# Kernel optimization log

Hardware: AMD Instinct MI355X
Metric: run time of the kernel (lower is better)

The kernel has to match this reference:

```python
import jax, jax.numpy as jnp
import numpy as np

B, L, D = 64, 512, 768          # batch, BERT seq len, BERT hidden
J = 31                          # clause boundaries per doc
S = J + 1                       # clauses per doc (= decoder max_len)
H = 100                         # enc/dec GRU hidden
NC = 10                         # num label classes
EMB = 50                        # label embedding dim


def setup_inputs() -> dict:
    key = jax.random.key(0)
    ks = jax.random.split(key, 24)
    sc = 0.05
    hidden_state = jax.random.normal(ks[0], (B, L, D), jnp.float32)
    # strictly increasing, non-zero boundaries -> every clause slice is non-empty
    stride = L // S  # 16
    bert_clause_b = jnp.tile(((jnp.arange(J) + 1) * stride)[None, :], (B, 1)).astype(jnp.int32)
    p = dict(
        hidden_state=hidden_state,
        bert_clause_b=bert_clause_b,
        fc5_w=sc * jax.random.normal(ks[1], (D, 1), jnp.float32),
        fc5_b=jnp.zeros((1,), jnp.float32),
        # encoder bi-GRU (input 768 -> hidden 100), torch gate order r,z,n
        enc_wih_f=sc * jax.random.normal(ks[2], (3 * H, D), jnp.float32),
        enc_whh_f=sc * jax.random.normal(ks[3], (3 * H, H), jnp.float32),
        enc_bih_f=jnp.zeros((3 * H,), jnp.float32),
        enc_bhh_f=jnp.zeros((3 * H,), jnp.float32),
        enc_wih_b=sc * jax.random.normal(ks[4], (3 * H, D), jnp.float32),
        enc_whh_b=sc * jax.random.normal(ks[5], (3 * H, H), jnp.float32),
        enc_bih_b=jnp.zeros((3 * H,), jnp.float32),
        enc_bhh_b=jnp.zeros((3 * H,), jnp.float32),
        emb=sc * jax.random.normal(ks[6], (NC, EMB), jnp.float32),
        lin1_w=sc * jax.random.normal(ks[7], (H, 2 * H), jnp.float32),
        lin1_b=jnp.zeros((H,), jnp.float32),
        dec_wih=sc * jax.random.normal(ks[8], (3 * H, EMB + H), jnp.float32),
        dec_whh=sc * jax.random.normal(ks[9], (3 * H, H), jnp.float32),
        dec_bih=jnp.zeros((3 * H,), jnp.float32),
        dec_bhh=jnp.zeros((3 * H,), jnp.float32),
        h2l_w=sc * jax.random.normal(ks[10], (NC, H), jnp.float32),
        h2l_b=jnp.zeros((NC,), jnp.float32),
    )
    return p


def _gru_cell(x, h, wih, whh, bih, bhh):
    gi = x @ wih.T + bih
    gh = h @ whh.T + bhh
    gir, giz, gin = jnp.split(gi, 3, axis=-1)
    ghr, ghz, ghn = jnp.split(gh, 3, axis=-1)
    r = jax.nn.sigmoid(gir + ghr)
    z = jax.nn.sigmoid(giz + ghz)
    n = jnp.tanh(gin + r * ghn)
    return (1.0 - z) * n + z * h


def _gru_scan(xs, h0, wih, whh, bih, bhh):
    # xs: [T, B, I]
    def step(h, x):
        h2 = _gru_cell(x, h, wih, whh, bih, bhh)
        return h2, h2
    return jax.lax.scan(step, h0, xs)


def reference(hidden_state, bert_clause_b, fc5_w, fc5_b,
              enc_wih_f, enc_whh_f, enc_bih_f, enc_bhh_f,
              enc_wih_b, enc_whh_b, enc_bih_b, enc_bhh_b,
              emb, lin1_w, lin1_b, dec_wih, dec_whh, dec_bih, dec_bhh,
              h2l_w, h2l_b):
    # ---- batched_index_select: per-clause softmax-weighted pooling ----
    t = jnp.arange(L)
    seg_id = jnp.sum(t[None, :, None] >= bert_clause_b[:, None, :], axis=-1)  # [B, L]
    scores = jnp.squeeze(hidden_state @ fc5_w, -1) + fc5_b[0]                  # [B, L]
    mask = seg_id[:, None, :] == jnp.arange(S)[None, :, None]                  # [B, S, L]
    logits = jnp.where(mask, scores[:, None, :], -jnp.inf)
    w = jax.nn.softmax(logits, axis=-1)                                        # [B, S, L]
    doc = jnp.einsum('bsl,bld->bsd', w, hidden_state)                          # [B, S, D]

    # ---- encoder bi-GRU ----
    xs = doc.transpose(1, 0, 2)  # [S, B, D]
    h0 = jnp.zeros((B, H), jnp.float32)
    hT_f, ys_f = _gru_scan(xs, h0, enc_wih_f, enc_whh_f, enc_bih_f, enc_bhh_f)
    _, ys_b = _gru_scan(xs[::-1], h0, enc_wih_b, enc_whh_b, enc_bih_b, enc_bhh_b)
    output1 = jnp.concatenate([ys_f, ys_b[::-1]], axis=-1)  # [S, B, 2H]

    # ---- decoder (greedy / testing=True path) ----
    lin = output1 @ lin1_w.T + lin1_b  # [S, B, H]

    def dec_step(carry, lin_t):
        h, prev = carry
        x = jnp.concatenate([emb[prev], lin_t], axis=-1)  # [B, EMB+H]
        h2 = _gru_cell(x, h, dec_wih, dec_whh, dec_bih, dec_bhh)
        logp = jax.nn.log_softmax(h2 @ h2l_w.T + h2l_b, axis=-1)  # [B, NC]
        nxt = jnp.argmax(logp, axis=-1).astype(jnp.int32)
        return (h2, nxt), logp

    init = (hT_f, jnp.zeros((B,), jnp.int32))
    _, outputs = jax.lax.scan(dec_step, init, lin)
    return outputs  # [S, B, NC] log-probs
```

## Files before the change

kernel.cpp:

```cpp
#include <hip/hip_runtime.h>
#include <hip/hip_bf16.h>
#include <math.h>

#define B_ 64
#define L_ 512
#define D_ 768
#define J_ 31
#define S_ 32
#define H_ 100
#define G3 300
#define NC_ 10
#define EMB_ 50

__device__ __forceinline__ float sigmoidf_(float x) { return 1.0f / (1.0f + __expf(-x)); }
__device__ __forceinline__ float tanhf_(float x) {
    float e = __expf(2.0f * x);
    return 1.0f - 2.0f / (e + 1.0f);
}
__device__ __forceinline__ float dot4f_(float4 a, float4 b) {
    return a.x * b.x + a.y * b.y + a.z * b.z + a.w * b.w;
}

typedef _Float16 half2_t __attribute__((ext_vector_type(2)));
__device__ __forceinline__ half2_t u_as_h2(unsigned u) { return __builtin_bit_cast(half2_t, u); }
__device__ __forceinline__ unsigned packh2(float a, float b) {
    half2_t p; p.x = (_Float16)a; p.y = (_Float16)b;
    return __builtin_bit_cast(unsigned, p);
}

__global__ __launch_bounds__(256) void pool_prep_kernel(
    const float* __restrict__ hs, const int* __restrict__ cb,
    const float* __restrict__ fc5w, const float* __restrict__ fc5b,
    float* __restrict__ doc,
    const float* __restrict__ dwih, const float* __restrict__ l1w,
    const float* __restrict__ l1b, const float* __restrict__ emb,
    const float* __restrict__ bih,
    float* __restrict__ W2, float* __restrict__ b2, float* __restrict__ tcg,
    const float* __restrict__ ewhf, const float* __restrict__ ewhb,
    const float* __restrict__ dwhh, unsigned* __restrict__ wpack)
{
    __shared__ __align__(16) float acc_s[4][D_];
    __shared__ float m_s[4], l_s[4];

    int bidx = blockIdx.x;
    int tid = threadIdx.x;

    if (bidx >= 2048) {
        if (bidx < 2348) {
            int n = bidx - 2048;
            __shared__ float dw_s[H_];
            int k = tid;
            if (k < H_) dw_s[k] = dwih[(size_t)n * 150 + 50 + k];
            __syncthreads();
            if (k < 200) {
                float acc = 0.f;
                for (int i = 0; i < H_; ++i) acc += dw_s[i] * l1w[(size_t)i * 200 + k];
                W2[(size_t)n * 200 + k] = acc;
            } else if (k == 200) {
                float acc = 0.f;
                for (int i = 0; i < H_; ++i) acc += dw_s[i] * l1b[i];
                b2[n] = acc;
            } else if (k < 211) {
                int c = k - 201;
                float acc = bih[n];
                const float* er = emb + c * EMB_;
                const float* wr = dwih + (size_t)n * 150;
                for (int e = 0; e < EMB_; ++e) acc += er[e] * wr[e];
                tcg[c * G3 + n] = acc;
            }
        } else {
            int m = bidx - 2348;
            const float* whh = (m == 0) ? ewhf : (m == 1) ? ewhb : dwhh;
            for (int t = tid; t < 400; t += 256) {
                int j = t >> 2, q = t & 3;
                unsigned* o = wpack + (size_t)m * 16000 + (size_t)t * 40;
#pragma unroll
                for (int d = 0; d < 13; ++d) {
                    int k = 2 * (13 * q + d);
                    float r0 = (k < H_) ? whh[j * H_ + k] : 0.f;
                    float r1 = (k + 1 < H_) ? whh[j * H_ + k + 1] : 0.f;
                    float z0 = (k < H_) ? whh[(100 + j) * H_ + k] : 0.f;
                    float z1 = (k + 1 < H_) ? whh[(100 + j) * H_ + k + 1] : 0.f;
                    float n0 = (k < H_) ? whh[(200 + j) * H_ + k] : 0.f;
                    float n1 = (k + 1 < H_) ? whh[(200 + j) * H_ + k + 1] : 0.f;
                    o[d]      = packh2(r0, r1);
                    o[13 + d] = packh2(z0, z1);
                    o[26 + d] = packh2(n0, n1);
                }
                o[39] = 0u;
            }
        }
        return;
    }

    int s = bidx >> 6, b = bidx & 63;
    int start = (s == 0) ? 0 : cb[b * J_ + s - 1];
    int end   = (s == J_) ? L_ : cb[b * J_ + s];
    int nt = end - start;
    int lane = tid & 63, wv = tid >> 6;

    if (nt <= 0) {
        for (int d = tid; d < D_; d += 256) doc[((size_t)s * B_ + b) * D_ + d] = 0.f;
        return;
    }

    float4 fwv[3];
#pragma unroll
    for (int i = 0; i < 3; ++i)
        fwv[i] = *(const float4*)(fc5w + 4 * lane + 256 * i);
    float bias = fc5b[0];

    const float* base = hs + ((size_t)b * L_ + start) * D_;
    float m = -INFINITY, l = 0.f;
    float4 acc[3];
#pragma unroll
    for (int i = 0; i < 3; ++i) acc[i] = make_float4(0.f, 0.f, 0.f, 0.f);

    for (int t = wv; t < nt; t += 4) {
        const float* row = base + (size_t)t * D_;
        float4 x0 = *(const float4*)(row + 4 * lane);
        float4 x1 = *(const float4*)(row + 4 * lane + 256);
        float4 x2 = *(const float4*)(row + 4 * lane + 512);
        float p = dot4f_(x0, fwv[0]) + dot4f_(x1, fwv[1]) + dot4f_(x2, fwv[2]);
#pragma unroll
        for (int off = 32; off; off >>= 1) p += __shfl_xor(p, off);
        p += bias;
        if (p > m) {
            float sc = __expf(m - p);
            l *= sc;
#pragma unroll
            for (int i = 0; i < 3; ++i) {
                acc[i].x *= sc; acc[i].y *= sc; acc[i].z *= sc; acc[i].w *= sc;
            }
            m = p;
        }
        float e = __expf(p - m);
        l += e;
        acc[0].x += e * x0.x; acc[0].y += e * x0.y; acc[0].z += e * x0.z; acc[0].w += e * x0.w;
        acc[1].x += e * x1.x; acc[1].y += e * x1.y; acc[1].z += e * x1.z; acc[1].w += e * x1.w;
        acc[2].x += e * x2.x; acc[2].y += e * x2.y; acc[2].z += e * x2.z; acc[2].w += e * x2.w;
    }
#pragma unroll
    for (int i = 0; i < 3; ++i)
        *(float4*)&acc_s[wv][4 * lane + 256 * i] = acc[i];
    if (lane == 0) { m_s[wv] = m; l_s[wv] = l; }
    __syncthreads();

    float M = fmaxf(fmaxf(m_s[0], m_s[1]), fmaxf(m_s[2], m_s[3]));
    float f0 = (l_s[0] > 0.f) ? __expf(m_s[0] - M) : 0.f;
    float f1 = (l_s[1] > 0.f) ? __expf(m_s[1] - M) : 0.f;
    float f2 = (l_s[2] > 0.f) ? __expf(m_s[2] - M) : 0.f;
    float f3 = (l_s[3] > 0.f) ? __expf(m_s[3] - M) : 0.f;
    float inv = 1.f / (l_s[0] * f0 + l_s[1] * f1 + l_s[2] * f2 + l_s[3] * f3);
    float* o = doc + ((size_t)s * B_ + b) * D_;
#pragma unroll
    for (int i = 0; i < 3; ++i) {
        int d = tid + 256 * i;
        float num = acc_s[0][d] * f0 + acc_s[1][d] * f1
                  + acc_s[2][d] * f2 + acc_s[3][d] * f3;
        o[d] = num * inv;
    }
}

__global__ __launch_bounds__(256) void gemm_enc(
    const float* __restrict__ A,
    const float* __restrict__ Wf, const float* __restrict__ Wb,
    const float* __restrict__ bf_, const float* __restrict__ bb_,
    float* __restrict__ C)
{
    __shared__ __align__(16) unsigned As[16][68];
    __shared__ __align__(16) unsigned Ws[16][68];
    int n0 = blockIdx.x * 64, m0 = blockIdx.y * 64;
    int tid = threadIdx.x;
    int tx = tid & 15, ty = tid >> 4;
    int lr = tid >> 2, lk4 = tid & 3;
    float acc[4][4] = {};

    for (int kk = 0; kk < 384; kk += 16) {
        {
            const float* ap = A + ((size_t)(m0 + lr)) * D_ + (kk + lk4 * 4) * 2;
            float4 x = *(const float4*)ap;
            float4 y = *(const float4*)(ap + 4);
            As[lk4 * 4 + 0][lr] = packh2(x.x, x.y);
            As[lk4 * 4 + 1][lr] = packh2(x.z, x.w);
            As[lk4 * 4 + 2][lr] = packh2(y.x, y.y);
            As[lk4 * 4 + 3][lr] = packh2(y.z, y.w);
            int n = n0 + lr;
            float4 u = make_float4(0.f, 0.f, 0.f, 0.f);
            float4 v = make_float4(0.f, 0.f, 0.f, 0.f);
            if (n < G3) {
                const float* wp = Wf + (size_t)n * D_ + (kk + lk4 * 4) * 2;
                u = *(const float4*)wp; v = *(const float4*)(wp + 4);
            } else if (n < 600) {
                const float* wp = Wb + (size_t)(n - G3) * D_ + (kk + lk4 * 4) * 2;
                u = *(const float4*)wp; v = *(const float4*)(wp + 4);
            }
            Ws[lk4 * 4 + 0][lr] = packh2(u.x, u.y);
            Ws[lk4 * 4 + 1][lr] = packh2(u.z, u.w);
            Ws[lk4 * 4 + 2][lr] = packh2(v.x, v.y);
            Ws[lk4 * 4 + 3][lr] = packh2(v.z, v.w);
        }
        __syncthreads();
#pragma unroll
        for (int ku = 0; ku < 16; ++ku) {
            uint4 av = *(const uint4*)&As[ku][ty * 4];
            uint4 wv = *(const uint4*)&Ws[ku][tx * 4];
            unsigned aa[4] = {av.x, av.y, av.z, av.w};
            unsigned ww[4] = {wv.x, wv.y, wv.z, wv.w};
#pragma unroll
            for (int i = 0; i < 4; ++i)
#pragma unroll
                for (int jj = 0; jj < 4; ++jj)
                    acc[i][jj] = __builtin_amdgcn_fdot2(u_as_h2(aa[i]), u_as_h2(ww[jj]),
                                                        acc[i][jj], false);
        }
        __syncthreads();
    }
#pragma unroll
    for (int jj = 0; jj < 4; ++jj) {
        int n = n0 + tx * 4 + jj;
        if (n >= 600) continue;
        float bias = (n < G3) ? bf_[n] : bb_[n - G3];
#pragma unroll
        for (int i = 0; i < 4; ++i) {
            int m = m0 + ty * 4 + i;
            C[(size_t)m * 600 + n] = acc[i][jj] + bias;
        }
    }
}

__global__ __launch_bounds__(256) void gemm_gil(
    const float* __restrict__ A, const float* __restrict__ W,
    const float* __restrict__ bias, float* __restrict__ C)
{
    __shared__ __align__(16) float As[16][68];
    __shared__ __align__(16) float Ws[16][68];
    int n0 = blockIdx.x * 64, m0 = blockIdx.y * 64;
    int tid = threadIdx.x;
    int tx = tid & 15, ty = tid >> 4;
    int lr = tid >> 2, lk4 = tid & 3;
    float acc[4][4] = {};

    for (int kk = 0; kk < 208; kk += 16) {
        int k = kk + lk4 * 4;
        float4 av = make_float4(0.f, 0.f, 0.f, 0.f);
        if (k < 200) av = *(const float4*)(A + (size_t)(m0 + lr) * 200 + k);
        As[lk4 * 4 + 0][lr] = av.x; As[lk4 * 4 + 1][lr] = av.y;
        As[lk4 * 4 + 2][lr] = av.z; As[lk4 * 4 + 3][lr] = av.w;
        int n = n0 + lr;
        float4 wv = make_float4(0.f, 0.f, 0.f, 0.f);
        if (n < G3 && k < 200) wv = *(const float4*)(W + (size_t)n * 200 + k);
        Ws[lk4 * 4 + 0][lr] = wv.x; Ws[lk4 * 4 + 1][lr] = wv.y;
        Ws[lk4 * 4 + 2][lr] = wv.z; Ws[lk4 * 4 + 3][lr] = wv.w;
        __syncthreads();
#pragma unroll
        for (int ki = 0; ki < 16; ++ki) {
            float4 a4 = *(const float4*)&As[ki][ty * 4];
            float4 w4 = *(const float4*)&Ws[ki][tx * 4];
            float ai[4] = {a4.x, a4.y, a4.z, a4.w};
            float wj[4] = {w4.x, w4.y, w4.z, w4.w};
#pragma unroll
            for (int i = 0; i < 4; ++i)
#pragma unroll
                for (int jj = 0; jj < 4; ++jj) acc[i][jj] += ai[i] * wj[jj];
        }
        __syncthreads();
    }
#pragma unroll
    for (int jj = 0; jj < 4; ++jj) {
        int n = n0 + tx * 4 + jj;
        if (n >= G3) continue;
#pragma unroll
        for (int i = 0; i < 4; ++i) {
            int m = m0 + ty * 4 + i;
            C[(size_t)m * G3 + n] = acc[i][jj] + bias[n];
        }
    }
}

#define LOAD_WREGS(WPBASE)                                                  \
    uint4 wq[10];                                                           \
    if (mv) {                                                               \
        const uint4* wp_ = (const uint4*)((WPBASE) + (size_t)tid * 40);     \
        _Pragma("unroll")                                                   \
        for (int i = 0; i < 10; ++i) wq[i] = wp_[i];                        \
    }

#define WD(i) (((i) & 3) == 0 ? wq[(i) >> 2].x : ((i) & 3) == 1 ? wq[(i) >> 2].y \
             : ((i) & 3) == 2 ? wq[(i) >> 2].z : wq[(i) >> 2].w)

#define MATVEC_REG(PBUF)                                                    \
    {                                                                       \
        const unsigned* hh = (const unsigned*)(PBUF);                       \
        _Pragma("unroll")                                                   \
        for (int d = 0; d < 13; ++d) {                                      \
            half2_t hv = u_as_h2(hh[13 * q + d]);                           \
            ar = __builtin_amdgcn_fdot2(u_as_h2(WD(d)),      hv, ar, false); \
            az = __builtin_amdgcn_fdot2(u_as_h2(WD(13 + d)), hv, az, false); \
            an = __builtin_amdgcn_fdot2(u_as_h2(WD(26 + d)), hv, an, false); \
        }                                                                   \
        ar += __shfl_xor(ar, 1); ar += __shfl_xor(ar, 2);                   \
        az += __shfl_xor(az, 1); az += __shfl_xor(az, 2);                   \
        an += __shfl_xor(an, 1); an += __shfl_xor(an, 2);                   \
    }

#define ENCT 448
#define ENC_SUB(GA0, GA1, GA2, NB0, NB1, NB2, SC, SN)                       \
    {                                                                       \
        if (mv) {                                                           \
            if (q == 0 && (SN) < S_) {                                      \
                int tn_ = bwd ? (S_ - 1 - (SN)) : (SN);                     \
                const float* gg_ = gi + ((size_t)tn_ * B_ + b) * 600 + goff; \
                NB0 = gg_[j]; NB1 = gg_[100 + j]; NB2 = gg_[200 + j];       \
            }                                                               \
            float ar = 0.f, az = 0.f, an = 0.f;                             \
            MATVEC_REG(hhalf[p])                                            \
            if (q == 0) {                                                   \
                int tc_ = bwd ? (S_ - 1 - (SC)) : (SC);                     \
                float r = sigmoidf_(GA0 + ar + bhr);                        \
                float z = sigmoidf_(GA1 + az + bhz);                        \
                float n = tanhf_(GA2 + r * (an + bhn));                     \
                float hn = (1.f - z) * n + z * hc;                          \
                hc = hn;                                                    \
                hhalf[p ^ 1][j] = (_Float16)hn;                             \
                out1[((size_t)tc_ * B_ + b) * 200 + ooff + j] = hn;         \
            }                                                               \
        }                                                                   \
        __syncthreads();                                                    \
        p ^= 1;                                                             \
    }

__global__ __launch_bounds__(ENCT, 1) void enc_scan(
    const float* __restrict__ gi, const unsigned* __restrict__ wpack,
    const float* __restrict__ bhh_f, const float* __restrict__ bhh_b,
    float* __restrict__ out1, float* __restrict__ hT)
{
    __shared__ __align__(8) _Float16 hhalf[2][104];

    int bid = blockIdx.x;
    int b = bid & 63;
    bool bwd = (bid >= 64);
    const float* bhh = bwd ? bhh_b : bhh_f;
    int tid = threadIdx.x;
    int j = tid >> 2, q = tid & 3;
    bool mv = tid < 400;
    const int goff = bwd ? G3 : 0;
    const int ooff = bwd ? H_ : 0;

    if (tid < 104) { hhalf[0][tid] = (_Float16)0.f; hhalf[1][tid] = (_Float16)0.f; }
    LOAD_WREGS(wpack + (bwd ? 16000 : 0))
    float bhr = 0.f, bhz = 0.f, bhn = 0.f, hc = 0.f;
    float pA0 = 0.f, pA1 = 0.f, pA2 = 0.f, pB0 = 0.f, pB1 = 0.f, pB2 = 0.f;
    if (mv && q == 0) {
        bhr = bhh[j]; bhz = bhh[100 + j]; bhn = bhh[200 + j];
        int t0 = bwd ? (S_ - 1) : 0;
        const float* gg = gi + ((size_t)t0 * B_ + b) * 600 + goff;
        pA0 = gg[j]; pA1 = gg[100 + j]; pA2 = gg[200 + j];
    }
    __syncthreads();

    int p = 0;
    for (int step = 0; step < S_; step += 2) {
        ENC_SUB(pA0, pA1, pA2, pB0, pB1, pB2, step, step + 1)
        ENC_SUB(pB0, pB1, pB2, pA0, pA1, pA2, step + 1, step + 2)
    }
    if (!bwd && mv && q == 0) hT[b * H_ + j] = hc;
}

#define DECT 448
#define DEC_LOGITS(TPREV)                                                   \
    {                                                                       \
        float acc_ = 0.f;                                                   \
        if (lane < 40) {                                                    \
            int c_ = lane >> 2, part_ = lane & 3;                           \
            const float* hr_ = hl_s + c_ * H_;                              \
            const float* hv_ = hf[p];                                       \
            int k0_ = 25 * part_;                                           \
            for (int k_ = k0_; k_ < k0_ + 25; ++k_) acc_ += hr_[k_] * hv_[k_]; \
            acc_ += __shfl_xor(acc_, 1);                                    \
            acc_ += __shfl_xor(acc_, 2);                                    \
        }                                                                   \
        float src_ = __shfl(acc_, (lane < NC_) ? 4 * lane : 0);             \
        float lv_ = (lane < NC_) ? src_ + hlb_r : -INFINITY;                \
        float mx_ = lv_; int am_ = lane & 15;                               \
        _Pragma("unroll")                                                   \
        for (int m_ = 8; m_; m_ >>= 1) {                                    \
            float ov_ = __shfl_xor(mx_, m_);                                \
            int oa_ = __shfl_xor(am_, m_);                                  \
            if (ov_ > mx_ || (ov_ == mx_ && oa_ < am_)) { mx_ = ov_; am_ = oa_; } \
        }                                                                   \
        if (w0) {                                                           \
            float e_ = (lane < NC_) ? __expf(lv_ - mx_) : 0.f;              \
            float se_ = e_;                                                 \
            _Pragma("unroll")                                               \
            for (int m_ = 8; m_; m_ >>= 1) se_ += __shfl_xor(se_, m_);      \
            if (lane < NC_) {                                               \
                float lse_ = mx_ + __logf(se_);                             \
                out[((size_t)(TPREV) * B_ + b) * NC_ + lane] = lv_ - lse_;  \
            }                                                               \
        }                                                                   \
        prev = __shfl(am_, 0);                                              \
    }

#define DEC_SUB(GA0, GA1, GA2, NB0, NB1, NB2, TC)                           \
    {                                                                       \
        float ar = 0.f, az = 0.f, an = 0.f;                                 \
        if (mv && (TC) < S_) {                                              \
            if (q == 0 && (TC) + 1 < S_) {                                  \
                const float* gg_ = gi_lin + ((size_t)((TC) + 1) * B_ + b) * G3; \
                NB0 = gg_[j]; NB1 = gg_[100 + j]; NB2 = gg_[200 + j];       \
            }                                                               \
            MATVEC_REG(hhalf[p])                                            \
        }                                                                   \
        if ((TC) >= 1) DEC_LOGITS((TC) - 1)                                 \
        if (mv && (TC) < S_ && q == 0) {                                    \
            const float* tcp_ = tc_s + prev * G3;                           \
            float r = sigmoidf_(GA0 + tcp_[j]       + ar + bhr);            \
            float z = sigmoidf_(GA1 + tcp_[100 + j] + az + bhz);            \
            float n = tanhf_(   GA2 + tcp_[200 + j] + r * (an + bhn));      \
            float hn = (1.f - z) * n + z * hc;                              \
            hc = hn;                                                        \
            hf[p ^ 1][j] = hn;                                              \
            hhalf[p ^ 1][j] = (_Float16)hn;                                 \
        }                                                                   \
        __syncthreads();                                                    \
        p ^= 1;                                                             \
    }

__global__ __launch_bounds__(DECT, 1) void dec_scan(
    const float* __restrict__ gi_lin, const unsigned* __restrict__ wpack,
    const float* __restrict__ bhh, const float* __restrict__ tcg,
    const float* __restrict__ h2lw, const float* __restrict__ h2lb,
    const float* __restrict__ hT, float* __restrict__ out)
{
    __shared__ float tc_s[NC_ * G3];
    __shared__ float hl_s[NC_ * H_];
    __shared__ __align__(8) _Float16 hhalf[2][104];
    __shared__ __align__(16) float hf[2][104];

    int bid = blockIdx.x;
    int b = bid & 63;
    int tid = threadIdx.x;
    int j = tid >> 2, q = tid & 3;
    bool mv = tid < 400;
    int lane = tid & 63;
    bool w0 = (tid < 64);

    for (int idx = tid; idx < NC_ * G3; idx += DECT) tc_s[idx] = tcg[idx];
    for (int idx = tid; idx < NC_ * H_; idx += DECT) hl_s[idx] = h2lw[idx];
    if (tid < 104) {
        float hv = (tid < H_) ? hT[b * H_ + tid] : 0.f;
        hf[0][tid] = hv;            hf[1][tid] = 0.f;
        hhalf[0][tid] = (_Float16)hv; hhalf[1][tid] = (_Float16)0.f;
    }
    LOAD_WREGS(wpack + 32000)
    float bhr = 0.f, bhz = 0.f, bhn = 0.f, hc = 0.f;
    float pA0 = 0.f, pA1 = 0.f, pA2 = 0.f, pB0 = 0.f, pB1 = 0.f, pB2 = 0.f;
    if (mv && q == 0) {
        bhr = bhh[j]; bhz = bhh[100 + j]; bhn = bhh[200 + j];
        hc = hT[b * H_ + j];
        const float* gg = gi_lin + ((size_t)0 * B_ + b) * G3;
        pA0 = gg[j]; pA1 = gg[100 + j]; pA2 = gg[200 + j];
    }
    float hlb_r = (lane < NC_) ? h2lb[lane] : 0.f;
    int prev = 0;
    __syncthreads();

    int p = 0;
    DEC_SUB(pA0, pA1, pA2, pB0, pB1, pB2, 0)
    for (int it = 0; it < 16; ++it) {
        int tA = 2 * it + 1, tB = 2 * it + 2;
        DEC_SUB(pB0, pB1, pB2, pA0, pA1, pA2, tA)
        DEC_SUB(pA0, pA1, pA2, pB0, pB1, pB2, tB)
    }
}

extern "C" void kernel_launch(void* const* d_in, const int* in_sizes, int n_in,
                              void* d_out, int out_size, void* d_ws, size_t ws_size,
                              hipStream_t stream)
{
    const float* hs   = (const float*)d_in[0];
    const int*   cb   = (const int*)  d_in[1];
    const float* fc5w = (const float*)d_in[2];
    const float* fc5b = (const float*)d_in[3];
    const float* ewif = (const float*)d_in[4];
    const float* ewhf = (const float*)d_in[5];
    const float* ebif = (const float*)d_in[6];
    const float* ebhf = (const float*)d_in[7];
    const float* ewib = (const float*)d_in[8];
    const float* ewhb = (const float*)d_in[9];
    const float* ebib = (const float*)d_in[10];
    const float* ebhb = (const float*)d_in[11];
    const float* emb  = (const float*)d_in[12];
    const float* l1w  = (const float*)d_in[13];
    const float* l1b  = (const float*)d_in[14];
    const float* dwih = (const float*)d_in[15];
    const float* dwhh = (const float*)d_in[16];
    const float* dbih = (const float*)d_in[17];
    const float* dbhh = (const float*)d_in[18];
    const float* h2lw = (const float*)d_in[19];
    const float* h2lb = (const float*)d_in[20];
    float* out = (float*)d_out;

    float* ws   = (float*)d_ws;
    float* doc  = ws;
    float* gi   = doc  + 1572864;
    float* out1 = gi   + 1228800;
    float* hT   = out1 + 409600;
    float* W2   = hT   + 6400;
    float* b2   = W2   + 60000;
    float* tcg  = b2   + 320;
    float* gil  = tcg  + 3072;
    unsigned* wpack = (unsigned*)(gil + 614400);

    pool_prep_kernel<<<2351, 256, 0, stream>>>(
        hs, cb, fc5w, fc5b, doc,
        dwih, l1w, l1b, emb, dbih, W2, b2, tcg,
        ewhf, ewhb, dwhh, wpack);
    gemm_enc<<<dim3(10, 32), 256, 0, stream>>>(doc, ewif, ewib, ebif, ebib, gi);
    enc_scan<<<128, ENCT, 0, stream>>>(gi, wpack, ebhf, ebhb, out1, hT);
    gemm_gil<<<dim3(5, 32), 256, 0, stream>>>(out1, W2, b2, gil);
    dec_scan<<<64, DECT, 0, stream>>>(gil, wpack, dbhh, tcg,
                                      h2lw, h2lb, hT, out);
}
```

Measured before the change: 169.4 us.

## Use MFMA f16 matrix cores for encoder input GEMM with fp16 staging

The pooling kernel now writes the clause document matrix as fp16, and extra blocks in the prep kernel convert both encoder input weight matrices into a padded fp16 buffer. The packed-dot shared-memory encoder GEMM is replaced by an MFMA 16x16x32 f16 kernel that loads A and B fragments directly from global memory, one 16x16 output tile per wave. This targets the scalar-dot GEMM cost and halves the bytes read for the document matrix. In exchange, the prep kernel grows by 152 weight-conversion blocks and there is no shared-memory reuse across waves.

```diff
diff --git a/kernel.cpp b/kernel.cpp
--- a/kernel.cpp
+++ b/kernel.cpp
@@ -22,6 +22,8 @@
 }
 
 typedef _Float16 half2_t __attribute__((ext_vector_type(2)));
+typedef _Float16 f16x8 __attribute__((ext_vector_type(8)));
+typedef float f32x4 __attribute__((ext_vector_type(4)));
 __device__ __forceinline__ half2_t u_as_h2(unsigned u) { return __builtin_bit_cast(half2_t, u); }
 __device__ __forceinline__ unsigned packh2(float a, float b) {
     half2_t p; p.x = (_Float16)a; p.y = (_Float16)b;
@@ -31,13 +33,15 @@
 __global__ __launch_bounds__(256) void pool_prep_kernel(
     const float* __restrict__ hs, const int* __restrict__ cb,
     const float* __restrict__ fc5w, const float* __restrict__ fc5b,
-    float* __restrict__ doc,
+    _Float16* __restrict__ doc_h,
     const float* __restrict__ dwih, const float* __restrict__ l1w,
     const float* __restrict__ l1b, const float* __restrict__ emb,
     const float* __restrict__ bih,
     float* __restrict__ W2, float* __restrict__ b2, float* __restrict__ tcg,
     const float* __restrict__ ewhf, const float* __restrict__ ewhb,
-    const float* __restrict__ dwhh, unsigned* __restrict__ wpack)
+    const float* __restrict__ dwhh, unsigned* __restrict__ wpack,
+    const float* __restrict__ ewif, const float* __restrict__ ewib,
+    _Float16* __restrict__ wh)
 {
     __shared__ __align__(16) float acc_s[4][D_];
     __shared__ float m_s[4], l_s[4];
@@ -68,7 +72,7 @@
                 for (int e = 0; e < EMB_; ++e) acc += er[e] * wr[e];
                 tcg[c * G3 + n] = acc;
             }
-        } else {
+        } else if (bidx < 2351) {
             int m = bidx - 2348;
             const float* whh = (m == 0) ? ewhf : (m == 1) ? ewhb : dwhh;
             for (int t = tid; t < 400; t += 256) {
@@ -89,6 +93,18 @@
                 }
                 o[39] = 0u;
             }
+        } else {
+            int ri = bidx - 2351;
+            for (int idx = tid; idx < 3072; idx += 256) {
+                int rr = idx >> 9;
+                rr = idx / 768;
+                int k = idx - rr * 768;
+                int n = 4 * ri + rr;
+                float v = 0.f;
+                if (n < G3) v = ewif[(size_t)n * D_ + k];
+                else if (n < 600) v = ewib[(size_t)(n - G3) * D_ + k];
+                wh[(size_t)n * D_ + k] = (_Float16)v;
+            }
         }
         return;
     }
@@ -100,7 +116,7 @@
     int lane = tid & 63, wv = tid >> 6;
 
     if (nt <= 0) {
-        for (int d = tid; d < D_; d += 256) doc[((size_t)s * B_ + b) * D_ + d] = 0.f;
+        for (int d = tid; d < D_; d += 256) doc_h[((size_t)s * B_ + b) * D_ + d] = (_Float16)0.f;
         return;
     }
 
@@ -152,79 +168,44 @@
     float f2 = (l_s[2] > 0.f) ? __expf(m_s[2] - M) : 0.f;
     float f3 = (l_s[3] > 0.f) ? __expf(m_s[3] - M) : 0.f;
     float inv = 1.f / (l_s[0] * f0 + l_s[1] * f1 + l_s[2] * f2 + l_s[3] * f3);
-    float* o = doc + ((size_t)s * B_ + b) * D_;
+    _Float16* o = doc_h + ((size_t)s * B_ + b) * D_;
 #pragma unroll
     for (int i = 0; i < 3; ++i) {
         int d = tid + 256 * i;
         float num = acc_s[0][d] * f0 + acc_s[1][d] * f1
                   + acc_s[2][d] * f2 + acc_s[3][d] * f3;
-        o[d] = num * inv;
-    }
-}
-
-__global__ __launch_bounds__(256) void gemm_enc(
-    const float* __restrict__ A,
-    const float* __restrict__ Wf, const float* __restrict__ Wb,
+        o[d] = (_Float16)(num * inv);
+    }
+}
+
+__global__ __launch_bounds__(256) void gemm_enc_mfma(
+    const _Float16* __restrict__ dh, const _Float16* __restrict__ wh,
     const float* __restrict__ bf_, const float* __restrict__ bb_,
     float* __restrict__ C)
 {
-    __shared__ __align__(16) unsigned As[16][68];
-    __shared__ __align__(16) unsigned Ws[16][68];
-    int n0 = blockIdx.x * 64, m0 = blockIdx.y * 64;
-    int tid = threadIdx.x;
-    int tx = tid & 15, ty = tid >> 4;
-    int lr = tid >> 2, lk4 = tid & 3;
-    float acc[4][4] = {};
-
-    for (int kk = 0; kk < 384; kk += 16) {
-        {
-            const float* ap = A + ((size_t)(m0 + lr)) * D_ + (kk + lk4 * 4) * 2;
-            float4 x = *(const float4*)ap;
-            float4 y = *(const float4*)(ap + 4);
-            As[lk4 * 4 + 0][lr] = packh2(x.x, x.y);
-            As[lk4 * 4 + 1][lr] = packh2(x.z, x.w);
-            As[lk4 * 4 + 2][lr] = packh2(y.x, y.y);
-            As[lk4 * 4 + 3][lr] = packh2(y.z, y.w);
-            int n = n0 + lr;
-            float4 u = make_float4(0.f, 0.f, 0.f, 0.f);
-            float4 v = make_float4(0.f, 0.f, 0.f, 0.f);
-            if (n < G3) {
-                const float* wp = Wf + (size_t)n * D_ + (kk + lk4 * 4) * 2;
-                u = *(const float4*)wp; v = *(const float4*)(wp + 4);
-            } else if (n < 600) {
-                const float* wp = Wb + (size_t)(n - G3) * D_ + (kk + lk4 * 4) * 2;
-                u = *(const float4*)wp; v = *(const float4*)(wp + 4);
-            }
-            Ws[lk4 * 4 + 0][lr] = packh2(u.x, u.y);
-            Ws[lk4 * 4 + 1][lr] = packh2(u.z, u.w);
-            Ws[lk4 * 4 + 2][lr] = packh2(v.x, v.y);
-            Ws[lk4 * 4 + 3][lr] = packh2(v.z, v.w);
-        }
-        __syncthreads();
-#pragma unroll
-        for (int ku = 0; ku < 16; ++ku) {
-            uint4 av = *(const uint4*)&As[ku][ty * 4];
-            uint4 wv = *(const uint4*)&Ws[ku][tx * 4];
-            unsigned aa[4] = {av.x, av.y, av.z, av.w};
-            unsigned ww[4] = {wv.x, wv.y, wv.z, wv.w};
-#pragma unroll
-            for (int i = 0; i < 4; ++i)
-#pragma unroll
-                for (int jj = 0; jj < 4; ++jj)
-                    acc[i][jj] = __builtin_amdgcn_fdot2(u_as_h2(aa[i]), u_as_h2(ww[jj]),
-                                                        acc[i][jj], false);
-        }
-        __syncthreads();
-    }
-#pragma unroll
-    for (int jj = 0; jj < 4; ++jj) {
-        int n = n0 + tx * 4 + jj;
-        if (n >= 600) continue;
-        float bias = (n < G3) ? bf_[n] : bb_[n - G3];
-#pragma unroll
-        for (int i = 0; i < 4; ++i) {
-            int m = m0 + ty * 4 + i;
-            C[(size_t)m * 600 + n] = acc[i][jj] + bias;
+    int w = threadIdx.x >> 6, l = threadIdx.x & 63;
+    int m0 = (blockIdx.y * 4 + w) * 16;
+    int n0 = blockIdx.x * 16;
+    int rowA = m0 + (l & 15);
+    int rowB = n0 + (l & 15);
+    int kb = (l >> 4) * 8;
+
+    const f16x8* ap = (const f16x8*)(dh + (size_t)rowA * D_ + kb);
+    const f16x8* bp = (const f16x8*)(wh + (size_t)rowB * D_ + kb);
+    f32x4 acc = {0.f, 0.f, 0.f, 0.f};
+#pragma unroll
+    for (int k = 0; k < 24; ++k) {
+        f16x8 a = ap[k * 4];
+        f16x8 b = bp[k * 4];
+        acc = __builtin_amdgcn_mfma_f32_16x16x32_f16(a, b, acc, 0, 0, 0);
+    }
+    int nc = n0 + (l & 15);
+    if (nc < 600) {
+        float bias = (nc < G3) ? bf_[nc] : bb_[nc - G3];
+#pragma unroll
+        for (int r = 0; r < 4; ++r) {
+            int mr = m0 + (l >> 4) * 4 + r;
+            C[(size_t)mr * 600 + nc] = acc[r] + bias;
         }
     }
 }
@@ -503,8 +484,9 @@
     float* out = (float*)d_out;
 
     float* ws   = (float*)d_ws;
-    float* doc  = ws;
-    float* gi   = doc  + 1572864;
+    _Float16* doc_h = (_Float16*)ws;
+    _Float16* wh    = (_Float16*)(ws + 800000);
+    float* gi   = ws + 1572864;
     float* out1 = gi   + 1228800;
     float* hT   = out1 + 409600;
     float* W2   = hT   + 6400;
@@ -513,11 +495,12 @@
     float* gil  = tcg  + 3072;
     unsigned* wpack = (unsigned*)(gil + 614400);
 
-    pool_prep_kernel<<<2351, 256, 0, stream>>>(
-        hs, cb, fc5w, fc5b, doc,
+    pool_prep_kernel<<<2503, 256, 0, stream>>>(
+        hs, cb, fc5w, fc5b, doc_h,
         dwih, l1w, l1b, emb, dbih, W2, b2, tcg,
-        ewhf, ewhb, dwhh, wpack);
-    gemm_enc<<<dim3(10, 32), 256, 0, stream>>>(doc, ewif, ewib, ebif, ebib, gi);
+        ewhf, ewhb, dwhh, wpack,
+        ewif, ewib, wh);
+    gemm_enc_mfma<<<dim3(38, 32), 256, 0, stream>>>(doc_h, wh, ebif, ebib, gi);
     enc_scan<<<128, ENCT, 0, stream>>>(gi, wpack, ebhf, ebhb, out1, hT);
     gemm_gil<<<dim3(5, 32), 256, 0, stream>>>(out1, W2, b2, gil);
     dec_scan<<<64, DECT, 0, stream>>>(gil, wpack, dbhh, tcg,
```

After: 159.2 us. -6.1%, faster.
